# Optimization experiments

Measured on AMD Instinct MI355X. Metric: run time of the kernel, lower is better.

Reference implementation:

```python
import jax, jax.numpy as jnp
import numpy as np

B, N, OBS, H, HEADS = 8192, 32, 128, 256, 4
HD = H // HEADS  # head dim = 64
GAIN = (0.125 / H) ** 0.5
LN_EPS = 1e-5


def _ln(x):
    # LayerNorm over last dim, no affine (elementwise_affine=False)
    m = x.mean(axis=-1, keepdims=True)
    v = ((x - m) ** 2).mean(axis=-1, keepdims=True)
    return (x - m) * jax.lax.rsqrt(v + LN_EPS)


def setup_inputs() -> dict:
    key = jax.random.key(0)
    ks = jax.random.split(key, 20)
    f32 = jnp.float32
    # weights stored (in, out) so y = x @ W + b (transpose of torch layout)
    def w(k, i, o, g):
        return (jax.random.normal(k, (i, o), dtype=f32) * g)
    inp = {
        "all_agent_obs": jax.random.normal(ks[0], (B, N, OBS), dtype=f32),
        # EntityEmbedding (obs-only): 1-layer LinearEncoder, normal init * t-fixup gain
        "W_emb": w(ks[1], OBS, H, GAIN), "b_emb": jnp.zeros((H,), f32),
        # ResidualSelfAttention projections
        "Wq": w(ks[2], H, H, GAIN), "bq": jnp.zeros((H,), f32),
        "Wk": w(ks[3], H, H, GAIN), "bk": jnp.zeros((H,), f32),
        "Wv": w(ks[4], H, H, GAIN), "bv": jnp.zeros((H,), f32),
        "Wo": w(ks[5], H, H, GAIN), "bo": jnp.zeros((H,), f32),
        # LinearEncoder tail (num_layers=2), kaiming-ish scale * t-fixup gain
        "W1": w(ks[6], H, H, GAIN), "b1": jnp.zeros((H,), f32),
        "W2": w(ks[7], H, H, GAIN), "b2": jnp.zeros((H,), f32),
        # value head: Linear(h_size + 1, 1)
        "Wval": w(ks[8], H + 1, 1, (1.0 / (H + 1)) ** 0.5), "bval": jnp.zeros((1,), f32),
    }
    return inp


def reference(all_agent_obs, W_emb, b_emb, Wq, bq, Wk, bk, Wv, bv, Wo, bo,
              W1, b1, W2, b2, Wval, bval):
    # --- EntityEmbedding: 1-layer MLP with SiLU ---
    ent = jax.nn.silu(jnp.einsum("bno,oh->bnh", all_agent_obs, W_emb) + b_emb)

    # --- ResidualSelfAttention (pre-norm, no mask) ---
    x = _ln(ent)                                        # embedding_norm
    q = (x @ Wq + bq).reshape(B, N, HEADS, HD)
    k = (x @ Wk + bk).reshape(B, N, HEADS, HD)
    v = (x @ Wv + bv).reshape(B, N, HEADS, HD)
    attn = jnp.einsum("bnhd,bmhd->bhnm", q, k) / jnp.sqrt(jnp.float32(HD))
    attn = jax.nn.softmax(attn, axis=-1)
    out = jnp.einsum("bhnm,bmhd->bnhd", attn, v).reshape(B, N, H)
    out = _ln(out @ Wo + bo + x)                        # fc_out + residual, residual_norm
    pooled = out.mean(axis=1)                           # (B, H) unmasked avg pool

    # --- LinearEncoder tail (2 layers, SiLU) ---
    enc = jax.nn.silu(pooled @ W1 + b1)
    enc = jax.nn.silu(enc @ W2 + b2)

    # --- norm agent count: max_agents updates to N, so val = N*2/N - 1 = 1.0 ---
    nc = jnp.ones((B, 1), dtype=enc.dtype)
    enc = jnp.concatenate([enc, nc], axis=-1)           # (B, H+1)
    return enc @ Wval + bval                            # (B, 1)
```

## Files before the change

kernel.cpp:

```cpp
#include <hip/hip_runtime.h>


typedef __bf16 bf16x8 __attribute__((ext_vector_type(8)));
typedef float f32x4 __attribute__((ext_vector_type(4)));
typedef unsigned short ushort_t;

#define DEVI static __device__ __forceinline__
#define MFMA16(a, b, cc) __builtin_amdgcn_mfma_f32_16x16x32_bf16((a), (b), (cc), 0, 0, 0)

#define WAITV2 asm volatile("s_waitcnt vmcnt(2)" ::: "memory")
#define WAITV0 asm volatile("s_waitcnt vmcnt(0)" ::: "memory")
#define WAITLG asm volatile("s_waitcnt lgkmcnt(0)" ::: "memory")
#define BAR() __builtin_amdgcn_s_barrier()

constexpr int OWemb_ = 0;
constexpr int OWq_   = 32768;
constexpr int OWk_   = OWq_ + 65536;
constexpr int OWv_   = OWk_ + 65536;
constexpr int OWo_   = OWv_ + 65536;
constexpr int OW1_   = OWo_ + 65536;
constexpr int OW2_   = OW1_ + 65536;

constexpr int OBS_STRIDE = 264;
constexpr int L_BST = 32768;
constexpr int L_PP  = 65536;
constexpr int LDS_TOTAL = 65536 + 2048;
static_assert(LDS_TOTAL <= 80 * 1024, "need <=80KB for 2 blocks/CU");

DEVI float silu_f(float x) { return x / (1.0f + __expf(-x)); }
DEVI f32x4 splat4(float x) { f32x4 v = {x, x, x, x}; return v; }
DEVI uint2 pack4(f32x4 v) {
  union { __bf16 h[4]; uint2 u; } x;
  x.h[0] = (__bf16)v[0]; x.h[1] = (__bf16)v[1];
  x.h[2] = (__bf16)v[2]; x.h[3] = (__bf16)v[3];
  return x.u;
}
DEVI f32x4 unpk(uint2 u) {
  union { uint2 u2; __bf16 h[4]; } x; x.u2 = u;
  f32x4 v = {(float)x.h[0], (float)x.h[1], (float)x.h[2], (float)x.h[3]};
  return v;
}
DEVI bf16x8 ld_frag(const char* p) { return *(const bf16x8*)p; }
DEVI bf16x8 u4b(unsigned a, unsigned b, unsigned cc, unsigned d) {
  union { unsigned u[4]; bf16x8 v; } x;
  x.u[0] = a; x.u[1] = b; x.u[2] = cc; x.u[3] = d;
  return x.v;
}
DEVI unsigned to_agpr(unsigned v) {
  unsigned d;
  asm volatile("v_accvgpr_write_b32 %0, %1" : "=a"(d) : "v"(v));
  return d;
}
DEVI unsigned from_agpr(unsigned a) {
  unsigned d;
  asm volatile("v_accvgpr_read_b32 %0, %1" : "=v"(d) : "a"(a));
  return d;
}
DEVI int xaddr(int row, int k4) {
  int t = row >> 4, cc = row & 15;
  int ks = k4 >> 5, kg = (k4 >> 3) & 3, half = (k4 >> 2) & 1;
  return ((t * 8 + ks) * 64 + kg * 16 + cc) * 16 + half * 8;
}

typedef const __attribute__((address_space(1))) unsigned int* gas_ptr;
typedef __attribute__((address_space(3))) unsigned int* las_ptr;
DEVI void gload16(const void* g, void* l) {
  __builtin_amdgcn_global_load_lds((gas_ptr)g, (las_ptr)l, 16, 0, 0);
}

constexpr int CSRC(int p) {
  return (p < 4)  ? (OWemb_ + p * 8192)
       : (p < 12) ? (OWq_ + (p - 4) * 8192)
       : (p < 20) ? (OWv_ + (p - 12) * 8192)
       : (p < 28) ? (OWk_ + (p - 20) * 8192)
                  : (OWo_ + (p - 28) * 8192);
}

DEVI void issue_chunk(const ushort_t* pw, int srcOff, char* bst, int slot, int wv, int lane) {
  char* dst = bst + slot * 16384 + wv * 2048;
  const ushort_t* s = pw + srcOff + wv * 1024 + (size_t)lane * 8;
  gload16(s, dst);
  gload16(s + 512, dst + 1024);
}
#define PH_ISSUE(p) issue_chunk(pw, CSRC(p), bst, (p) & 1, wv, lane)

__global__ void pack_weights(const float* __restrict__ Wemb, const float* __restrict__ Wq,
                             const float* __restrict__ Wk, const float* __restrict__ Wv,
                             const float* __restrict__ Wo, const float* __restrict__ W1,
                             const float* __restrict__ W2, ushort_t* __restrict__ ws) {
  int t = blockIdx.x * 256 + threadIdx.x;
  if (t >= 53248) return;
  const float* src;
  int dst, n, k0;
  if (t < 4096) {
    int rem = t & 1023;
    int ctg = rem >> 6, l = rem & 63;
    n = ctg * 16 + (l & 15);
    k0 = (t >> 10) * 32 + (l >> 4) * 8;
    src = Wemb; dst = OWemb_ + t * 8;
  } else if (t < 36864) {
    int u = t - 4096, m = u >> 13, loc = u & 8191;
    int rem = loc & 1023;
    int ctg = rem >> 6, l = rem & 63;
    n = ctg * 16 + (l & 15);
    k0 = (loc >> 10) * 32 + (l >> 4) * 8;
    src = (m == 0) ? Wq : (m == 1) ? Wk : (m == 2) ? Wv : Wo;
    dst = OWq_ + m * 65536 + loc * 8;
  } else {
    int u = t - 36864, m = u >> 13, loc = u & 8191;
    int ln = loc & 63, ks = (loc >> 6) & 7, ct = loc >> 9;
    n = ct * 16 + (ln & 15);
    k0 = ks * 32 + (ln >> 4) * 8;
    src = m ? W2 : W1; dst = OW1_ + m * 65536 + loc * 8;
  }
  union { __bf16 h[8]; uint4 u; } pk;
  #pragma unroll
  for (int j = 0; j < 8; ++j) pk.h[j] = (__bf16)src[(k0 + j) * 256 + n];
  *(uint4*)(ws + dst) = pk.u;
}

__global__ __launch_bounds__(512, 4)
void poca_fused(const float* __restrict__ obs, const ushort_t* __restrict__ pw,
                const float* __restrict__ b_emb, const float* __restrict__ bq,
                const float* __restrict__ bk, const float* __restrict__ bv,
                const float* __restrict__ bo, const float* __restrict__ b1,
                const float* __restrict__ b2, const float* __restrict__ Wval,
                const float* __restrict__ bval, float* __restrict__ out) {
  __shared__ __align__(128) char lds[LDS_TOTAL];
  const int tid = threadIdx.x;
  const int wv = tid >> 6, lane = tid & 63;
  const int g = lane >> 4, c = lane & 15;
  const int mg = wv >> 2, ng = wv & 3;
  char* xb = lds;
  char* bst = lds + L_BST;
  char* as_ = bst + wv * 4096;
  char* ppb = lds + L_PP;
  char* poolb = bst;
  char* y1b = bst + 8448;
  char* ptlb = bst + 16896;

  PH_ISSUE(0);

  {
    const float4* op = (const float4*)(obs + (size_t)blockIdx.x * 64 * 128);
    #pragma unroll
    for (int it = 0; it < 4; ++it) {
      int idx = it * 512 + tid;
      float4 v = op[idx];
      int row = idx >> 5, col4 = idx & 31;
      union { __bf16 h[4]; uint2 u; } cv;
      cv.h[0] = (__bf16)v.x; cv.h[1] = (__bf16)v.y;
      cv.h[2] = (__bf16)v.z; cv.h[3] = (__bf16)v.w;
      *(uint2*)(xb + row * OBS_STRIDE + col4 * 8) = cv.u;
    }
  }
  WAITLG;

  f32x4 acc[2][4];

  #pragma unroll
  for (int p = 0; p < 4; ++p) {
    PH_ISSUE(p + 1); WAITV2; BAR();
    if (p == 0) {
      #pragma unroll
      for (int ct = 0; ct < 4; ++ct) {
        f32x4 b_ = *(const f32x4*)(b_emb + ng * 64 + ct * 16 + g * 4);
        acc[0][ct] = b_; acc[1][ct] = b_;
      }
    }
    const char* ck = bst + (p & 1) * 16384;
    bf16x8 wf[4], xf[2];
    #pragma unroll
    for (int t = 0; t < 4; ++t) wf[t] = ld_frag(ck + ((ng * 4 + t) * 64 + lane) * 16);
    #pragma unroll
    for (int rt = 0; rt < 2; ++rt)
      xf[rt] = ld_frag(xb + ((mg * 2 + rt) * 16 + c) * OBS_STRIDE + p * 64 + g * 16);
    #pragma unroll
    for (int rt = 0; rt < 2; ++rt)
      #pragma unroll
      for (int ct = 0; ct < 4; ++ct) acc[rt][ct] = MFMA16(wf[ct], xf[rt], acc[rt][ct]);
    WAITLG; BAR();
  }

  #pragma unroll
  for (int rt = 0; rt < 2; ++rt)
    #pragma unroll
    for (int ct = 0; ct < 4; ++ct)
      #pragma unroll
      for (int r = 0; r < 4; ++r) acc[rt][ct][r] = silu_f(acc[rt][ct][r]);
  #pragma unroll
  for (int rt = 0; rt < 2; ++rt) {
    float s1 = 0.f, s2 = 0.f;
    #pragma unroll
    for (int ct = 0; ct < 4; ++ct)
      #pragma unroll
      for (int r = 0; r < 4; ++r) { float e = acc[rt][ct][r]; s1 += e; s2 += e * e; }
    s1 += __shfl_xor(s1, 16); s2 += __shfl_xor(s2, 16);
    s1 += __shfl_xor(s1, 32); s2 += __shfl_xor(s2, 32);
    if (g == 0)
      *(float2*)(ppb + (mg * 32 + rt * 16 + c) * 32 + ng * 8) = make_float2(s1, s2);
  }
  WAITLG; BAR();
  {
    float mu[2], rs[2];
    #pragma unroll
    for (int rt = 0; rt < 2; ++rt) {
      int row = mg * 32 + rt * 16 + c;
      f32x4 pA = *(const f32x4*)(ppb + row * 32);
      f32x4 pB = *(const f32x4*)(ppb + row * 32 + 16);
      float S1 = pA[0] + pA[2] + pB[0] + pB[2];
      float S2 = pA[1] + pA[3] + pB[1] + pB[3];
      float m_ = S1 * (1.f / 256.f);
      float v_ = S2 * (1.f / 256.f) - m_ * m_;
      mu[rt] = m_; rs[rt] = rsqrtf(v_ + 1e-5f);
    }
    #pragma unroll
    for (int rt = 0; rt < 2; ++rt)
      #pragma unroll
      for (int ct = 0; ct < 4; ++ct) {
        f32x4 xv;
        #pragma unroll
        for (int r = 0; r < 4; ++r) xv[r] = (acc[rt][ct][r] - mu[rt]) * rs[rt];
        *(uint2*)(xb + xaddr(mg * 32 + rt * 16 + c, ng * 64 + ct * 16 + g * 4)) = pack4(xv);
      }
  }
  WAITLG; BAR();

  #pragma unroll
  for (int p = 4; p < 12; ++p) {
    PH_ISSUE(p + 1); WAITV2; BAR();
    if (p == 4) {
      #pragma unroll
      for (int ct = 0; ct < 4; ++ct) {
        f32x4 b_ = *(const f32x4*)(bq + ng * 64 + ct * 16 + g * 4);
        acc[0][ct] = b_; acc[1][ct] = b_;
      }
    }
    const char* ck = bst + (p & 1) * 16384;
    const int ks = p - 4;
    bf16x8 wf[4], xf[2];
    #pragma unroll
    for (int t = 0; t < 4; ++t) wf[t] = ld_frag(ck + ((ng * 4 + t) * 64 + lane) * 16);
    #pragma unroll
    for (int rt = 0; rt < 2; ++rt)
      xf[rt] = ld_frag(xb + (((mg * 2 + rt) * 8 + ks) * 64 + lane) * 16);
    #pragma unroll
    for (int rt = 0; rt < 2; ++rt)
      #pragma unroll
      for (int ct = 0; ct < 4; ++ct) acc[rt][ct] = MFMA16(wf[ct], xf[rt], acc[rt][ct]);
    WAITLG; BAR();
  }

  unsigned qs[16];
  #pragma unroll
  for (int rt = 0; rt < 2; ++rt)
    #pragma unroll
    for (int ct = 0; ct < 4; ++ct) {
      uint2 qp = pack4(acc[rt][ct]);
      qs[(rt * 4 + ct) * 2] = to_agpr(qp.x);
      qs[(rt * 4 + ct) * 2 + 1] = to_agpr(qp.y);
    }

  #pragma unroll
  for (int p = 12; p < 20; ++p) {
    PH_ISSUE(p + 1); WAITV2; BAR();
    if (p == 12) {
      #pragma unroll
      for (int ct = 0; ct < 4; ++ct) {
        f32x4 b_ = splat4(bv[ng * 64 + ct * 16 + c]);
        acc[0][ct] = b_; acc[1][ct] = b_;
      }
    }
    const char* ck = bst + (p & 1) * 16384;
    const int ks = p - 12;
    bf16x8 wf[4], xf[2];
    #pragma unroll
    for (int t = 0; t < 4; ++t) wf[t] = ld_frag(ck + ((ng * 4 + t) * 64 + lane) * 16);
    #pragma unroll
    for (int rt = 0; rt < 2; ++rt)
      xf[rt] = ld_frag(xb + (((mg * 2 + rt) * 8 + ks) * 64 + lane) * 16);
    #pragma unroll
    for (int rt = 0; rt < 2; ++rt)
      #pragma unroll
      for (int ct = 0; ct < 4; ++ct) acc[rt][ct] = MFMA16(xf[rt], wf[ct], acc[rt][ct]);
    WAITLG; BAR();
  }

  unsigned vs[16];
  #pragma unroll
  for (int rt = 0; rt < 2; ++rt)
    #pragma unroll
    for (int ct = 0; ct < 4; ++ct) {
      uint2 vp = pack4(acc[rt][ct]);
      vs[(rt * 4 + ct) * 2] = to_agpr(vp.x);
      vs[(rt * 4 + ct) * 2 + 1] = to_agpr(vp.y);
    }

  #pragma unroll
  for (int p = 20; p < 28; ++p) {
    if (p < 27) { PH_ISSUE(p + 1); WAITV2; } else { WAITV0; }
    BAR();
    if (p == 20) {
      #pragma unroll
      for (int ct = 0; ct < 4; ++ct) {
        f32x4 b_ = *(const f32x4*)(bk + ng * 64 + ct * 16 + g * 4);
        acc[0][ct] = b_; acc[1][ct] = b_;
      }
    }
    const char* ck = bst + (p & 1) * 16384;
    const int ks = p - 20;
    bf16x8 wf[4], xf[2];
    #pragma unroll
    for (int t = 0; t < 4; ++t) wf[t] = ld_frag(ck + ((ng * 4 + t) * 64 + lane) * 16);
    #pragma unroll
    for (int rt = 0; rt < 2; ++rt)
      xf[rt] = ld_frag(xb + (((mg * 2 + rt) * 8 + ks) * 64 + lane) * 16);
    #pragma unroll
    for (int rt = 0; rt < 2; ++rt)
      #pragma unroll
      for (int ct = 0; ct < 4; ++ct) acc[rt][ct] = MFMA16(wf[ct], xf[rt], acc[rt][ct]);
    WAITLG; BAR();
  }

  {
    f32x4 sacc[2][2];
    sacc[0][0] = splat4(0.f); sacc[0][1] = splat4(0.f);
    sacc[1][0] = splat4(0.f); sacc[1][1] = splat4(0.f);
    #pragma unroll
    for (int hf = 0; hf < 2; ++hf) {
      #pragma unroll
      for (int rt2 = 0; rt2 < 2; ++rt2)
        #pragma unroll
        for (int ctl = 0; ctl < 2; ++ctl) {
          int gr = ctl * 2 + (g >> 1);
          int off = rt2 * 1024 + (gr * 16 + c) * 16 + (g & 1) * 8;
          int qi = (rt2 * 4 + hf * 2 + ctl) * 2;
          *(uint2*)(as_ + off) = make_uint2(from_agpr(qs[qi]), from_agpr(qs[qi + 1]));
          *(uint2*)(as_ + 2048 + off) = pack4(acc[rt2][hf * 2 + ctl]);
        }
      WAITLG;
      bf16x8 qf[2], kf[2];
      #pragma unroll
      for (int t = 0; t < 2; ++t) {
        qf[t] = ld_frag(as_ + t * 1024 + lane * 16);
        kf[t] = ld_frag(as_ + 2048 + t * 1024 + lane * 16);
      }
      #pragma unroll
      for (int qt = 0; qt < 2; ++qt)
        #pragma unroll
        for (int kt = 0; kt < 2; ++kt)
          sacc[qt][kt] = MFMA16(kf[kt], qf[qt], sacc[qt][kt]);
    }
    float rinv[2];
    uint2 p_pk[2][2];
    #pragma unroll
    for (int qt = 0; qt < 2; ++qt) {
      float sc[2][4];
      float mx = -3e38f;
      #pragma unroll
      for (int kt = 0; kt < 2; ++kt)
        #pragma unroll
        for (int r = 0; r < 4; ++r) { sc[kt][r] = sacc[qt][kt][r] * 0.125f; mx = fmaxf(mx, sc[kt][r]); }
      mx = fmaxf(mx, __shfl_xor(mx, 16));
      mx = fmaxf(mx, __shfl_xor(mx, 32));
      float sm = 0.f;
      #pragma unroll
      for (int kt = 0; kt < 2; ++kt)
        #pragma unroll
        for (int r = 0; r < 4; ++r) { float e = __expf(sc[kt][r] - mx); sc[kt][r] = e; sm += e; }
      sm += __shfl_xor(sm, 16);
      sm += __shfl_xor(sm, 32);
      rinv[qt] = 1.0f / sm;
      #pragma unroll
      for (int kt = 0; kt < 2; ++kt) {
        f32x4 pv = {sc[kt][0], sc[kt][1], sc[kt][2], sc[kt][3]};
        p_pk[qt][kt] = pack4(pv);
      }
    }
    #pragma unroll
    for (int rt2 = 0; rt2 < 2; ++rt2)
      #pragma unroll
      for (int ct = 0; ct < 4; ++ct) {
        int gr = rt2 * 2 + (g >> 1);
        int off = ct * 1024 + (gr * 16 + c) * 16 + (g & 1) * 8;
        int vi = (rt2 * 4 + ct) * 2;
        *(uint2*)(as_ + off) = make_uint2(from_agpr(vs[vi]), from_agpr(vs[vi + 1]));
      }
    uint2 respk[2][4];
    #pragma unroll
    for (int rt = 0; rt < 2; ++rt)
      #pragma unroll
      for (int ct = 0; ct < 4; ++ct)
        respk[rt][ct] = *(uint2*)(xb + xaddr(mg * 32 + rt * 16 + c, ng * 64 + ct * 16 + g * 4));
    WAITLG;
    bf16x8 vf[4];
    #pragma unroll
    for (int dt = 0; dt < 4; ++dt) vf[dt] = ld_frag(as_ + dt * 1024 + lane * 16);
    const int l1 = (g & 1) * 32 + c, l2 = l1 + 16;
    const bool hi = (g >= 2);
    #pragma unroll
    for (int qt = 0; qt < 2; ++qt) {
      unsigned x0k0 = __shfl(p_pk[qt][0].x, l1), x0k1 = __shfl(p_pk[qt][1].x, l1);
      unsigned y0k0 = __shfl(p_pk[qt][0].y, l1), y0k1 = __shfl(p_pk[qt][1].y, l1);
      unsigned x1k0 = __shfl(p_pk[qt][0].x, l2), x1k1 = __shfl(p_pk[qt][1].x, l2);
      unsigned y1k0 = __shfl(p_pk[qt][0].y, l2), y1k1 = __shfl(p_pk[qt][1].y, l2);
      bf16x8 pf = u4b(hi ? x0k1 : x0k0, hi ? y0k1 : y0k0, hi ? x1k1 : x1k0, hi ? y1k1 : y1k0);
      #pragma unroll
      for (int dt = 0; dt < 4; ++dt) {
        f32x4 o = splat4(0.f);
        o = MFMA16(vf[dt], pf, o);
        #pragma unroll
        for (int r = 0; r < 4; ++r) o[r] *= rinv[qt];
        *(uint2*)(xb + xaddr(mg * 32 + qt * 16 + c, ng * 64 + dt * 16 + g * 4)) = pack4(o);
      }
    }
    #pragma unroll
    for (int ct = 0; ct < 4; ++ct) {
      f32x4 b_ = *(const f32x4*)(bo + ng * 64 + ct * 16 + g * 4);
      #pragma unroll
      for (int rt = 0; rt < 2; ++rt) acc[rt][ct] = b_ + unpk(respk[rt][ct]);
    }
  }
  WAITLG; BAR();
  PH_ISSUE(28);

  #pragma unroll
  for (int p = 28; p < 36; ++p) {
    if (p < 35) { PH_ISSUE(p + 1); WAITV2; } else { WAITV0; }
    BAR();
    const char* ck = bst + (p & 1) * 16384;
    const int ks = p - 28;
    bf16x8 wf[4], xf[2];
    #pragma unroll
    for (int t = 0; t < 4; ++t) wf[t] = ld_frag(ck + ((ng * 4 + t) * 64 + lane) * 16);
    #pragma unroll
    for (int rt = 0; rt < 2; ++rt)
      xf[rt] = ld_frag(xb + (((mg * 2 + rt) * 8 + ks) * 64 + lane) * 16);
    #pragma unroll
    for (int rt = 0; rt < 2; ++rt)
      #pragma unroll
      for (int ct = 0; ct < 4; ++ct) acc[rt][ct] = MFMA16(wf[ct], xf[rt], acc[rt][ct]);
    WAITLG; BAR();
  }

  #pragma unroll
  for (int rt = 0; rt < 2; ++rt) {
    float s1 = 0.f, s2 = 0.f;
    #pragma unroll
    for (int ct = 0; ct < 4; ++ct)
      #pragma unroll
      for (int r = 0; r < 4; ++r) { float e = acc[rt][ct][r]; s1 += e; s2 += e * e; }
    s1 += __shfl_xor(s1, 16); s2 += __shfl_xor(s2, 16);
    s1 += __shfl_xor(s1, 32); s2 += __shfl_xor(s2, 32);
    if (g == 0)
      *(float2*)(ppb + (mg * 32 + rt * 16 + c) * 32 + ng * 8) = make_float2(s1, s2);
  }
  WAITLG; BAR();
  {
    float mu[2], rs[2];
    #pragma unroll
    for (int rt = 0; rt < 2; ++rt) {
      int row = mg * 32 + rt * 16 + c;
      f32x4 pA = *(const f32x4*)(ppb + row * 32);
      f32x4 pB = *(const f32x4*)(ppb + row * 32 + 16);
      float S1 = pA[0] + pA[2] + pB[0] + pB[2];
      float S2 = pA[1] + pA[3] + pB[1] + pB[3];
      float m_ = S1 * (1.f / 256.f);
      float v_ = S2 * (1.f / 256.f) - m_ * m_;
      mu[rt] = m_; rs[rt] = rsqrtf(v_ + 1e-5f);
    }
    f32x4 ps[4];
    #pragma unroll
    for (int ct = 0; ct < 4; ++ct) {
      #pragma unroll
      for (int r = 0; r < 4; ++r)
        ps[ct][r] = (acc[0][ct][r] - mu[0]) * rs[0] + (acc[1][ct][r] - mu[1]) * rs[1];
    }
    #pragma unroll
    for (int st = 1; st < 16; st <<= 1)
      #pragma unroll
      for (int ct = 0; ct < 4; ++ct)
        #pragma unroll
        for (int r = 0; r < 4; ++r) ps[ct][r] += __shfl_xor(ps[ct][r], st);
    if (c == 0) {
      #pragma unroll
      for (int ct = 0; ct < 4; ++ct) {
        f32x4 pv;
        #pragma unroll
        for (int r = 0; r < 4; ++r) pv[r] = ps[ct][r] * (1.f / 32.f);
        *(uint2*)(poolb + mg * 528 + (ng * 64 + ct * 16 + g * 4) * 2) = pack4(pv);
      }
    }
  }
  #pragma unroll
  for (int it = 0; it < 4; ++it) {
    int idx = it * 512 + tid;
    if (idx < 1792) {
      int row = 2 + (idx >> 7), col = idx & 127;
      *(unsigned*)(poolb + row * 528 + col * 4) = 0;
      *(unsigned*)(y1b + row * 528 + col * 4) = 0;
    }
  }
  WAITLG; BAR();

  f32x4 t1[2];
  #pragma unroll
  for (int ctl = 0; ctl < 2; ++ctl) t1[ctl] = splat4(b1[wv * 32 + ctl * 16 + c]);
  #pragma unroll
  for (int ks = 0; ks < 8; ++ks) {
    bf16x8 a = ld_frag(poolb + c * 528 + ks * 64 + g * 16);
    #pragma unroll
    for (int ctl = 0; ctl < 2; ++ctl) {
      bf16x8 b = *(const bf16x8*)(pw + OW1_ + (size_t)(((wv * 2 + ctl) * 8 + ks) * 64 + lane) * 8);
      t1[ctl] = MFMA16(a, b, t1[ctl]);
    }
  }
  if (g == 0) {
    #pragma unroll
    for (int ctl = 0; ctl < 2; ++ctl)
      #pragma unroll
      for (int r = 0; r < 4; ++r)
        *(__bf16*)(y1b + r * 528 + (wv * 32 + ctl * 16 + c) * 2) = (__bf16)silu_f(t1[ctl][r]);
  }
  WAITLG; BAR();
  f32x4 t2[2];
  #pragma unroll
  for (int ctl = 0; ctl < 2; ++ctl) t2[ctl] = splat4(b2[wv * 32 + ctl * 16 + c]);
  #pragma unroll
  for (int ks = 0; ks < 8; ++ks) {
    bf16x8 a = ld_frag(y1b + c * 528 + ks * 64 + g * 16);
    #pragma unroll
    for (int ctl = 0; ctl < 2; ++ctl) {
      bf16x8 b = *(const bf16x8*)(pw + OW2_ + (size_t)(((wv * 2 + ctl) * 8 + ks) * 64 + lane) * 8);
      t2[ctl] = MFMA16(a, b, t2[ctl]);
    }
  }
  if (g == 0) {
    float part[4] = {0.f, 0.f, 0.f, 0.f};
    #pragma unroll
    for (int ctl = 0; ctl < 2; ++ctl) {
      float wvv = Wval[wv * 32 + ctl * 16 + c];
      #pragma unroll
      for (int r = 0; r < 4; ++r) part[r] += silu_f(t2[ctl][r]) * wvv;
    }
    #pragma unroll
    for (int m = 1; m < 16; m <<= 1) {
      #pragma unroll
      for (int r = 0; r < 4; ++r) part[r] += __shfl_xor(part[r], m);
    }
    if (c == 0) {
      float4 p4 = make_float4(part[0], part[1], part[2], part[3]);
      *(float4*)(ptlb + wv * 16) = p4;
    }
  }
  WAITLG; BAR();
  if (tid < 2) {
    float s = Wval[256] + bval[0];
    const float* pt = (const float*)ptlb;
    #pragma unroll
    for (int w8 = 0; w8 < 8; ++w8) s += pt[w8 * 4 + tid];
    out[(size_t)blockIdx.x * 2 + tid] = s;
  }
}

extern "C" void kernel_launch(void* const* d_in, const int* in_sizes, int n_in,
                              void* d_out, int out_size, void* d_ws, size_t ws_size,
                              hipStream_t stream) {
  (void)in_sizes; (void)n_in; (void)out_size; (void)ws_size;
  const float* obs  = (const float*)d_in[0];
  const float* Wemb = (const float*)d_in[1];
  const float* bemb = (const float*)d_in[2];
  const float* Wq   = (const float*)d_in[3];
  const float* bq   = (const float*)d_in[4];
  const float* Wk   = (const float*)d_in[5];
  const float* bk   = (const float*)d_in[6];
  const float* Wv   = (const float*)d_in[7];
  const float* bv   = (const float*)d_in[8];
  const float* Wo   = (const float*)d_in[9];
  const float* bo   = (const float*)d_in[10];
  const float* W1   = (const float*)d_in[11];
  const float* b1   = (const float*)d_in[12];
  const float* W2   = (const float*)d_in[13];
  const float* b2   = (const float*)d_in[14];
  const float* Wval = (const float*)d_in[15];
  const float* bval = (const float*)d_in[16];
  ushort_t* ws = (ushort_t*)d_ws;
  float* out = (float*)d_out;

  pack_weights<<<208, 256, 0, stream>>>(Wemb, Wq, Wk, Wv, Wo, W1, W2, ws);
  poca_fused<<<4096, 512, 0, stream>>>(obs, ws, bemb, bq, bk, bv, bo, b1, b2, Wval, bval, out);
}
```

Before: 332.9 us.

## Triple-buffer weight chunks and drop per-step barrier in GEMM loops

Moves weight staging from a double buffer to a triple buffer, with prefetch distance two, and removes the trailing LDS wait and barrier from each k-step so only one barrier per step remains. It also reorders the projections to compute K before attention and V afterwards, which removes the AGPR stash of V, and hoists bias loads ahead of the barriers. LDS use grows to 80KB, which may limit occupancy, and the LayerNorm scratch is now aliased into the staging buffers, so correctness depends on the barrier placement.

```diff
diff --git a/kernel.cpp b/kernel.cpp
--- a/kernel.cpp
+++ b/kernel.cpp
@@ -12,6 +12,7 @@
 #define WAITV0 asm volatile("s_waitcnt vmcnt(0)" ::: "memory")
 #define WAITLG asm volatile("s_waitcnt lgkmcnt(0)" ::: "memory")
 #define BAR() __builtin_amdgcn_s_barrier()
+#define SCHEDB() __builtin_amdgcn_sched_barrier(0)
 
 constexpr int OWemb_ = 0;
 constexpr int OWq_   = 32768;
@@ -23,9 +24,8 @@
 
 constexpr int OBS_STRIDE = 264;
 constexpr int L_BST = 32768;
-constexpr int L_PP  = 65536;
-constexpr int LDS_TOTAL = 65536 + 2048;
-static_assert(LDS_TOTAL <= 80 * 1024, "need <=80KB for 2 blocks/CU");
+constexpr int LDS_TOTAL = 32768 + 3 * 16384;
+static_assert(LDS_TOTAL <= 81920, "need <=80KB for 2 blocks/CU");
 
 DEVI float silu_f(float x) { return x / (1.0f + __expf(-x)); }
 DEVI f32x4 splat4(float x) { f32x4 v = {x, x, x, x}; return v; }
@@ -71,8 +71,8 @@
 constexpr int CSRC(int p) {
   return (p < 4)  ? (OWemb_ + p * 8192)
        : (p < 12) ? (OWq_ + (p - 4) * 8192)
-       : (p < 20) ? (OWv_ + (p - 12) * 8192)
-       : (p < 28) ? (OWk_ + (p - 20) * 8192)
+       : (p < 20) ? (OWk_ + (p - 12) * 8192)
+       : (p < 28) ? (OWv_ + (p - 20) * 8192)
                   : (OWo_ + (p - 28) * 8192);
 }
 
@@ -82,7 +82,7 @@
   gload16(s, dst);
   gload16(s + 512, dst + 1024);
 }
-#define PH_ISSUE(p) issue_chunk(pw, CSRC(p), bst, (p) & 1, wv, lane)
+#define PH_ISSUE(ch) issue_chunk(pw, CSRC(ch), bst, (ch) % 3, wv, lane)
 
 __global__ void pack_weights(const float* __restrict__ Wemb, const float* __restrict__ Wq,
                              const float* __restrict__ Wk, const float* __restrict__ Wv,
@@ -134,12 +134,16 @@
   char* xb = lds;
   char* bst = lds + L_BST;
   char* as_ = bst + wv * 4096;
-  char* ppb = lds + L_PP;
+  char* pp1 = bst;
   char* poolb = bst;
   char* y1b = bst + 8448;
   char* ptlb = bst + 16896;
-
-  PH_ISSUE(0);
+  char* pp2 = bst + 20480;
+
+  PH_ISSUE(0); PH_ISSUE(1);
+  f32x4 bemb_r[4];
+  #pragma unroll
+  for (int ct = 0; ct < 4; ++ct) bemb_r[ct] = *(const f32x4*)(b_emb + ng * 64 + ct * 16 + g * 4);
 
   {
     const float4* op = (const float4*)(obs + (size_t)blockIdx.x * 64 * 128);
@@ -160,15 +164,13 @@
 
   #pragma unroll
   for (int p = 0; p < 4; ++p) {
-    PH_ISSUE(p + 1); WAITV2; BAR();
+    WAITV2; BAR();
+    PH_ISSUE(p + 2);
     if (p == 0) {
       #pragma unroll
-      for (int ct = 0; ct < 4; ++ct) {
-        f32x4 b_ = *(const f32x4*)(b_emb + ng * 64 + ct * 16 + g * 4);
-        acc[0][ct] = b_; acc[1][ct] = b_;
-      }
-    }
-    const char* ck = bst + (p & 1) * 16384;
+      for (int ct = 0; ct < 4; ++ct) { acc[0][ct] = bemb_r[ct]; acc[1][ct] = bemb_r[ct]; }
+    }
+    const char* ck = bst + (p % 3) * 16384;
     bf16x8 wf[4], xf[2];
     #pragma unroll
     for (int t = 0; t < 4; ++t) wf[t] = ld_frag(ck + ((ng * 4 + t) * 64 + lane) * 16);
@@ -179,9 +181,10 @@
     for (int rt = 0; rt < 2; ++rt)
       #pragma unroll
       for (int ct = 0; ct < 4; ++ct) acc[rt][ct] = MFMA16(wf[ct], xf[rt], acc[rt][ct]);
-    WAITLG; BAR();
-  }
-
+    SCHEDB();
+  }
+
+  BAR();
   #pragma unroll
   for (int rt = 0; rt < 2; ++rt)
     #pragma unroll
@@ -198,7 +201,7 @@
     s1 += __shfl_xor(s1, 16); s2 += __shfl_xor(s2, 16);
     s1 += __shfl_xor(s1, 32); s2 += __shfl_xor(s2, 32);
     if (g == 0)
-      *(float2*)(ppb + (mg * 32 + rt * 16 + c) * 32 + ng * 8) = make_float2(s1, s2);
+      *(float2*)(pp1 + (mg * 32 + rt * 16 + c) * 32 + ng * 8) = make_float2(s1, s2);
   }
   WAITLG; BAR();
   {
@@ -206,8 +209,8 @@
     #pragma unroll
     for (int rt = 0; rt < 2; ++rt) {
       int row = mg * 32 + rt * 16 + c;
-      f32x4 pA = *(const f32x4*)(ppb + row * 32);
-      f32x4 pB = *(const f32x4*)(ppb + row * 32 + 16);
+      f32x4 pA = *(const f32x4*)(pp1 + row * 32);
+      f32x4 pB = *(const f32x4*)(pp1 + row * 32 + 16);
       float S1 = pA[0] + pA[2] + pB[0] + pB[2];
       float S2 = pA[1] + pA[3] + pB[1] + pB[3];
       float m_ = S1 * (1.f / 256.f);
@@ -224,19 +227,21 @@
         *(uint2*)(xb + xaddr(mg * 32 + rt * 16 + c, ng * 64 + ct * 16 + g * 4)) = pack4(xv);
       }
   }
+  f32x4 bq_r[4];
+  #pragma unroll
+  for (int ct = 0; ct < 4; ++ct) bq_r[ct] = *(const f32x4*)(bq + ng * 64 + ct * 16 + g * 4);
+  SCHEDB();
   WAITLG; BAR();
 
   #pragma unroll
   for (int p = 4; p < 12; ++p) {
-    PH_ISSUE(p + 1); WAITV2; BAR();
+    WAITV2; BAR();
+    PH_ISSUE(p + 2);
     if (p == 4) {
       #pragma unroll
-      for (int ct = 0; ct < 4; ++ct) {
-        f32x4 b_ = *(const f32x4*)(bq + ng * 64 + ct * 16 + g * 4);
-        acc[0][ct] = b_; acc[1][ct] = b_;
-      }
-    }
-    const char* ck = bst + (p & 1) * 16384;
+      for (int ct = 0; ct < 4; ++ct) { acc[0][ct] = bq_r[ct]; acc[1][ct] = bq_r[ct]; }
+    }
+    const char* ck = bst + (p % 3) * 16384;
     const int ks = p - 4;
     bf16x8 wf[4], xf[2];
     #pragma unroll
@@ -248,7 +253,7 @@
     for (int rt = 0; rt < 2; ++rt)
       #pragma unroll
       for (int ct = 0; ct < 4; ++ct) acc[rt][ct] = MFMA16(wf[ct], xf[rt], acc[rt][ct]);
-    WAITLG; BAR();
+    SCHEDB();
   }
 
   unsigned qs[16];
@@ -260,18 +265,20 @@
       qs[(rt * 4 + ct) * 2] = to_agpr(qp.x);
       qs[(rt * 4 + ct) * 2 + 1] = to_agpr(qp.y);
     }
+  f32x4 bk_r[4];
+  #pragma unroll
+  for (int ct = 0; ct < 4; ++ct) bk_r[ct] = *(const f32x4*)(bk + ng * 64 + ct * 16 + g * 4);
 
   #pragma unroll
   for (int p = 12; p < 20; ++p) {
-    PH_ISSUE(p + 1); WAITV2; BAR();
+    if (p < 19) { WAITV2; } else { WAITV0; }
+    BAR();
+    if (p <= 17) PH_ISSUE(p + 2);
     if (p == 12) {
       #pragma unroll
-      for (int ct = 0; ct < 4; ++ct) {
-        f32x4 b_ = splat4(bv[ng * 64 + ct * 16 + c]);
-        acc[0][ct] = b_; acc[1][ct] = b_;
-      }
-    }
-    const char* ck = bst + (p & 1) * 16384;
+      for (int ct = 0; ct < 4; ++ct) { acc[0][ct] = bk_r[ct]; acc[1][ct] = bk_r[ct]; }
+    }
+    const char* ck = bst + (p % 3) * 16384;
     const int ks = p - 12;
     bf16x8 wf[4], xf[2];
     #pragma unroll
@@ -282,47 +289,15 @@
     #pragma unroll
     for (int rt = 0; rt < 2; ++rt)
       #pragma unroll
-      for (int ct = 0; ct < 4; ++ct) acc[rt][ct] = MFMA16(xf[rt], wf[ct], acc[rt][ct]);
-    WAITLG; BAR();
-  }
-
-  unsigned vs[16];
-  #pragma unroll
-  for (int rt = 0; rt < 2; ++rt)
-    #pragma unroll
-    for (int ct = 0; ct < 4; ++ct) {
-      uint2 vp = pack4(acc[rt][ct]);
-      vs[(rt * 4 + ct) * 2] = to_agpr(vp.x);
-      vs[(rt * 4 + ct) * 2 + 1] = to_agpr(vp.y);
-    }
-
-  #pragma unroll
-  for (int p = 20; p < 28; ++p) {
-    if (p < 27) { PH_ISSUE(p + 1); WAITV2; } else { WAITV0; }
+      for (int ct = 0; ct < 4; ++ct) acc[rt][ct] = MFMA16(wf[ct], xf[rt], acc[rt][ct]);
+    SCHEDB();
+  }
+
+  float rinv[2];
+  uint2 p_pk[2][2];
+  float bv_r[4];
+  {
     BAR();
-    if (p == 20) {
-      #pragma unroll
-      for (int ct = 0; ct < 4; ++ct) {
-        f32x4 b_ = *(const f32x4*)(bk + ng * 64 + ct * 16 + g * 4);
-        acc[0][ct] = b_; acc[1][ct] = b_;
-      }
-    }
-    const char* ck = bst + (p & 1) * 16384;
-    const int ks = p - 20;
-    bf16x8 wf[4], xf[2];
-    #pragma unroll
-    for (int t = 0; t < 4; ++t) wf[t] = ld_frag(ck + ((ng * 4 + t) * 64 + lane) * 16);
-    #pragma unroll
-    for (int rt = 0; rt < 2; ++rt)
-      xf[rt] = ld_frag(xb + (((mg * 2 + rt) * 8 + ks) * 64 + lane) * 16);
-    #pragma unroll
-    for (int rt = 0; rt < 2; ++rt)
-      #pragma unroll
-      for (int ct = 0; ct < 4; ++ct) acc[rt][ct] = MFMA16(wf[ct], xf[rt], acc[rt][ct]);
-    WAITLG; BAR();
-  }
-
-  {
     f32x4 sacc[2][2];
     sacc[0][0] = splat4(0.f); sacc[0][1] = splat4(0.f);
     sacc[1][0] = splat4(0.f); sacc[1][1] = splat4(0.f);
@@ -351,8 +326,6 @@
         for (int kt = 0; kt < 2; ++kt)
           sacc[qt][kt] = MFMA16(kf[kt], qf[qt], sacc[qt][kt]);
     }
-    float rinv[2];
-    uint2 p_pk[2][2];
     #pragma unroll
     for (int qt = 0; qt < 2; ++qt) {
       float sc[2][4];
@@ -378,13 +351,48 @@
       }
     }
     #pragma unroll
+    for (int ct = 0; ct < 4; ++ct) bv_r[ct] = bv[ng * 64 + ct * 16 + c];
+  }
+  SCHEDB();
+  WAITLG; BAR();
+  PH_ISSUE(20); PH_ISSUE(21);
+
+  #pragma unroll
+  for (int p = 20; p < 28; ++p) {
+    if (p < 27) { WAITV2; } else { WAITV0; }
+    BAR();
+    if (p <= 25) PH_ISSUE(p + 2);
+    if (p == 20) {
+      #pragma unroll
+      for (int ct = 0; ct < 4; ++ct) {
+        f32x4 b_ = splat4(bv_r[ct]);
+        acc[0][ct] = b_; acc[1][ct] = b_;
+      }
+    }
+    const char* ck = bst + (p % 3) * 16384;
+    const int ks = p - 20;
+    bf16x8 wf[4], xf[2];
+    #pragma unroll
+    for (int t = 0; t < 4; ++t) wf[t] = ld_frag(ck + ((ng * 4 + t) * 64 + lane) * 16);
+    #pragma unroll
+    for (int rt = 0; rt < 2; ++rt)
+      xf[rt] = ld_frag(xb + (((mg * 2 + rt) * 8 + ks) * 64 + lane) * 16);
+    #pragma unroll
+    for (int rt = 0; rt < 2; ++rt)
+      #pragma unroll
+      for (int ct = 0; ct < 4; ++ct) acc[rt][ct] = MFMA16(xf[rt], wf[ct], acc[rt][ct]);
+    SCHEDB();
+  }
+
+  {
+    BAR();
+    #pragma unroll
     for (int rt2 = 0; rt2 < 2; ++rt2)
       #pragma unroll
       for (int ct = 0; ct < 4; ++ct) {
         int gr = rt2 * 2 + (g >> 1);
         int off = ct * 1024 + (gr * 16 + c) * 16 + (g & 1) * 8;
-        int vi = (rt2 * 4 + ct) * 2;
-        *(uint2*)(as_ + off) = make_uint2(from_agpr(vs[vi]), from_agpr(vs[vi + 1]));
+        *(uint2*)(as_ + off) = pack4(acc[rt2][ct]);
       }
     uint2 respk[2][4];
     #pragma unroll
@@ -392,6 +400,9 @@
       #pragma unroll
       for (int ct = 0; ct < 4; ++ct)
         respk[rt][ct] = *(uint2*)(xb + xaddr(mg * 32 + rt * 16 + c, ng * 64 + ct * 16 + g * 4));
+    f32x4 bo_r[4];
+    #pragma unroll
+    for (int ct = 0; ct < 4; ++ct) bo_r[ct] = *(const f32x4*)(bo + ng * 64 + ct * 16 + g * 4);
     WAITLG;
     bf16x8 vf[4];
     #pragma unroll
@@ -416,19 +427,20 @@
     }
     #pragma unroll
     for (int ct = 0; ct < 4; ++ct) {
-      f32x4 b_ = *(const f32x4*)(bo + ng * 64 + ct * 16 + g * 4);
-      #pragma unroll
-      for (int rt = 0; rt < 2; ++rt) acc[rt][ct] = b_ + unpk(respk[rt][ct]);
-    }
-  }
-  WAITLG; BAR();
-  PH_ISSUE(28);
+      #pragma unroll
+      for (int rt = 0; rt < 2; ++rt) acc[rt][ct] = bo_r[ct] + unpk(respk[rt][ct]);
+    }
+  }
+  SCHEDB();
+  WAITLG; BAR();
+  PH_ISSUE(28); PH_ISSUE(29);
 
   #pragma unroll
   for (int p = 28; p < 36; ++p) {
-    if (p < 35) { PH_ISSUE(p + 1); WAITV2; } else { WAITV0; }
+    if (p < 35) { WAITV2; } else { WAITV0; }
     BAR();
-    const char* ck = bst + (p & 1) * 16384;
+    if (p <= 33) PH_ISSUE(p + 2);
+    const char* ck = bst + (p % 3) * 16384;
     const int ks = p - 28;
     bf16x8 wf[4], xf[2];
     #pragma unroll
@@ -440,9 +452,10 @@
     for (int rt = 0; rt < 2; ++rt)
       #pragma unroll
       for (int ct = 0; ct < 4; ++ct) acc[rt][ct] = MFMA16(wf[ct], xf[rt], acc[rt][ct]);
-    WAITLG; BAR();
-  }
-
+    SCHEDB();
+  }
+
+  BAR();
   #pragma unroll
   for (int rt = 0; rt < 2; ++rt) {
     float s1 = 0.f, s2 = 0.f;
@@ -453,7 +466,7 @@
     s1 += __shfl_xor(s1, 16); s2 += __shfl_xor(s2, 16);
     s1 += __shfl_xor(s1, 32); s2 += __shfl_xor(s2, 32);
     if (g == 0)
-      *(float2*)(ppb + (mg * 32 + rt * 16 + c) * 32 + ng * 8) = make_float2(s1, s2);
+      *(float2*)(pp2 + (mg * 32 + rt * 16 + c) * 32 + ng * 8) = make_float2(s1, s2);
   }
   WAITLG; BAR();
   {
@@ -461,8 +474,8 @@
     #pragma unroll
     for (int rt = 0; rt < 2; ++rt) {
       int row = mg * 32 + rt * 16 + c;
-      f32x4 pA = *(const f32x4*)(ppb + row * 32);
-      f32x4 pB = *(const f32x4*)(ppb + row * 32 + 16);
+      f32x4 pA = *(const f32x4*)(pp2 + row * 32);
+      f32x4 pB = *(const f32x4*)(pp2 + row * 32 + 16);
       float S1 = pA[0] + pA[2] + pB[0] + pB[2];
       float S2 = pA[1] + pA[3] + pB[1] + pB[3];
       float m_ = S1 * (1.f / 256.f);
```

After: 320.1 us. -3.8%, faster.
